# Optimization experiments

Measured on AMD Instinct MI355X. Metric: run time of the kernel, lower is better.

## Reference

```python
import jax, jax.numpy as jnp
import numpy as np

D, B, N, DIM, H, DH, MLP = 6, 4, 1024, 768, 12, 64, 3072
SCALE = DH ** -0.5
EPS = 1e-5


def setup_inputs() -> dict:
    key = jax.random.key(0)
    ks = jax.random.split(key, 5)
    s = 0.02
    return {
        "x": jax.random.normal(ks[0], (B, N, DIM), jnp.float32),
        "ln1_g": jnp.ones((D, DIM), jnp.float32),
        "ln1_b": jnp.zeros((D, DIM), jnp.float32),
        "wqkv": jax.random.normal(ks[1], (D, DIM, 3 * H * DH), jnp.float32) * s,
        "wo": jax.random.normal(ks[2], (D, H * DH, DIM), jnp.float32) * s,
        "bo": jnp.zeros((D, DIM), jnp.float32),
        "ln2_g": jnp.ones((D, DIM), jnp.float32),
        "ln2_b": jnp.zeros((D, DIM), jnp.float32),
        "w1": jax.random.normal(ks[3], (D, DIM, MLP), jnp.float32) * s,
        "b1": jnp.zeros((D, MLP), jnp.float32),
        "w2": jax.random.normal(ks[4], (D, MLP, DIM), jnp.float32) * s,
        "b2": jnp.zeros((D, DIM), jnp.float32),
    }


def _ln(h, g, b):
    m = h.mean(-1, keepdims=True)
    v = h.var(-1, keepdims=True)  # biased, matches torch LayerNorm
    return (h - m) / jnp.sqrt(v + EPS) * g + b


def _heads(t):
    # [b, n, h*d] -> [b, h, n, d]
    return t.reshape(B, N, H, DH).transpose(0, 2, 1, 3)


def reference(x, ln1_g, ln1_b, wqkv, wo, bo, ln2_g, ln2_b, w1, b1, w2, b2):
    def step(carry, p):
        xc, _, _ = carry
        g1, be1, Wqkv, Wo, Bo, g2, be2, W1, B1, W2, B2 = p
        h = _ln(xc, g1, be1)
        q, k, v = jnp.split(h @ Wqkv, 3, axis=-1)
        q, k, v = _heads(q), _heads(k), _heads(v)
        attn = jax.nn.softmax(jnp.einsum('bhid,bhjd->bhij', q, k) * SCALE, axis=-1)
        out = jnp.einsum('bhij,bhjd->bhid', attn, v)
        out = out.transpose(0, 2, 1, 3).reshape(B, N, H * DH)
        xc = xc + out @ Wo + Bo
        h2 = _ln(xc, g2, be2)
        xc = xc + jax.nn.gelu(h2 @ W1 + B1, approximate=False) @ W2 + B2
        return (xc, k, v), None

    kv0 = jnp.zeros((B, H, N, DH), x.dtype)
    (xf, k, v), _ = jax.lax.scan(
        step, (x, kv0, kv0),
        (ln1_g, ln1_b, wqkv, wo, bo, ln2_g, ln2_b, w1, b1, w2, b2))
    return xf, k, v
```

## Files before the change

kernel.cpp:

```cpp
#include <hip/hip_runtime.h>
#include <hip/hip_bf16.h>
#include <math.h>

typedef __bf16 bf16;
typedef __bf16 bf16x8 __attribute__((ext_vector_type(8)));
typedef float f32x4 __attribute__((ext_vector_type(4)));

enum { EPI_QKV = 0, EPI_GELU = 1 };

__device__ __forceinline__ void gload16(const void* g, void* s) {
  __builtin_amdgcn_global_load_lds((__attribute__((address_space(1))) void*)g,
                                   (__attribute__((address_space(3))) void*)s, 16, 0, 0);
}

#define MFMA16(a, b, c) __builtin_amdgcn_mfma_f32_16x16x32_bf16((a), (b), (c), 0, 0, 0)

__device__ __forceinline__ void xcd_swizzle(int& bx, int& by) {
  const int gx = gridDim.x, nwg = gx * gridDim.y;
  int bid = blockIdx.y * gx + blockIdx.x;
  if ((nwg & 7) == 0) bid = (bid & 7) * (nwg >> 3) + (bid >> 3);
  bx = bid % gx;
  by = bid / gx;
}

__global__ __launch_bounds__(256) void cast_x(const float* __restrict__ x,
                                              float* __restrict__ xq) {
  const int i = (blockIdx.x * 256 + threadIdx.x) * 4;
  float4 v = *(const float4*)(x + i);
  v.x = (float)(bf16)v.x; v.y = (float)(bf16)v.y;
  v.z = (float)(bf16)v.z; v.w = (float)(bf16)v.w;
  *(float4*)(xq + i) = v;
}

__global__ __launch_bounds__(256) void wconv_all(
    const float* __restrict__ wqkv, const float* __restrict__ wo,
    const float* __restrict__ w1, const float* __restrict__ w2,
    bf16* __restrict__ qkvT, bf16* __restrict__ woT,
    bf16* __restrict__ w1T, bf16* __restrict__ w2T, int lfix) {
  __shared__ float tile[32][33];
  const int bid = blockIdx.x;
  int l, r;
  if (lfix < 0) { l = bid / 6912; r = bid % 6912; } else { l = lfix; r = bid; }
  const int lo = (lfix < 0) ? l : 0;
  const float* W; bf16* Wt; int K, N, tt;
  if (r < 1728)      { W = wqkv + (size_t)l * 768 * 2304; Wt = qkvT + (size_t)lo * 2304 * 768; K = 768;  N = 2304; tt = r; }
  else if (r < 2304) { W = wo   + (size_t)l * 768 * 768;  Wt = woT  + (size_t)lo * 768 * 768;  K = 768;  N = 768;  tt = r - 1728; }
  else if (r < 4608) { W = w1   + (size_t)l * 768 * 3072; Wt = w1T  + (size_t)lo * 3072 * 768; K = 768;  N = 3072; tt = r - 2304; }
  else               { W = w2   + (size_t)l * 3072 * 768; Wt = w2T  + (size_t)lo * 768 * 3072; K = 3072; N = 768;  tt = r - 4608; }
  const int ntx = N >> 5;
  const int n0 = (tt % ntx) * 32, k0 = (tt / ntx) * 32;
  const int tx = threadIdx.x & 31, ty = threadIdx.x >> 5;
#pragma unroll
  for (int rr = 0; rr < 4; ++rr)
    tile[ty + rr * 8][tx] = W[(size_t)(k0 + ty + rr * 8) * N + n0 + tx];
  __syncthreads();
#pragma unroll
  for (int rr = 0; rr < 4; ++rr)
    Wt[(size_t)(n0 + ty + rr * 8) * K + k0 + tx] = (bf16)tile[tx][ty + rr * 8];
}

__global__ __launch_bounds__(256) void ln_kernel(const float* __restrict__ x,
                                                 const float* __restrict__ g,
                                                 const float* __restrict__ b,
                                                 bf16* __restrict__ out) {
  const int row = blockIdx.x, t = threadIdx.x;
  const float* xr = x + (size_t)row * 768;
  float v0 = xr[t], v1 = xr[t + 256], v2 = xr[t + 512];
  float s = v0 + v1 + v2, sq = v0 * v0 + v1 * v1 + v2 * v2;
#pragma unroll
  for (int m = 32; m; m >>= 1) { s += __shfl_xor(s, m); sq += __shfl_xor(sq, m); }
  __shared__ float rs[4], rq[4];
  const int w = t >> 6;
  if ((t & 63) == 0) { rs[w] = s; rq[w] = sq; }
  __syncthreads();
  s = rs[0] + rs[1] + rs[2] + rs[3];
  sq = rq[0] + rq[1] + rq[2] + rq[3];
  const float mean = s * (1.f / 768.f);
  const float var = sq * (1.f / 768.f) - mean * mean;
  const float rstd = rsqrtf(var + 1e-5f);
  bf16* orow = out + (size_t)row * 768;
  orow[t]       = (bf16)((v0 - mean) * rstd * g[t]       + b[t]);
  orow[t + 256] = (bf16)((v1 - mean) * rstd * g[t + 256] + b[t + 256]);
  orow[t + 512] = (bf16)((v2 - mean) * rstd * g[t + 512] + b[t + 512]);
}

template <int EPI>
__global__ __launch_bounds__(256) void gemm_s(
    const bf16* __restrict__ A, const bf16* __restrict__ Bt,
    const float* __restrict__ bias, bf16* __restrict__ Cb,
    bf16* __restrict__ qo, bf16* __restrict__ ko_, bf16* __restrict__ vo,
    float* __restrict__ kf, float* __restrict__ vf, int wf,
    int M, int Nc, int K) {
  __shared__ __align__(16) char lds[2][2][8192];
  const int t = threadIdx.x, lane = t & 63, w = t >> 6;
  const int wr = w >> 1, wc = w & 1;
  int bx, by;
  xcd_swizzle(bx, by);
  const size_t m0 = (size_t)by * 128, n0 = (size_t)bx * 128;

  const char* ab[2]; const char* bb[2];
#pragma unroll
  for (int r = 0; r < 2; ++r) {
    int c = r * 256 + t;
    ab[r] = (const char*)(A + (m0 + (c >> 2)) * (size_t)K) + (c & 3) * 16;
    bb[r] = (const char*)(Bt + (n0 + (c >> 2)) * (size_t)K) + (c & 3) * 16;
  }

  f32x4 acc[4][4] = {};

  auto stage = [&](int buf, int tt) {
#pragma unroll
    for (int r = 0; r < 2; ++r) {
      gload16(ab[r] + (size_t)tt * 64, &lds[buf][0][r * 4096 + w * 1024]);
      gload16(bb[r] + (size_t)tt * 64, &lds[buf][1][r * 4096 + w * 1024]);
    }
  };
  auto compute = [&](int buf) {
    const char* As = lds[buf][0];
    const char* Bs = lds[buf][1];
    const int ko = (lane >> 4) * 16;
    bf16x8 af[4], fb[4];
#pragma unroll
    for (int i = 0; i < 4; ++i) {
      af[i] = *(const bf16x8*)(As + (wr * 64 + i * 16 + (lane & 15)) * 64 + ko);
      fb[i] = *(const bf16x8*)(Bs + (wc * 64 + i * 16 + (lane & 15)) * 64 + ko);
    }
#pragma unroll
    for (int mi = 0; mi < 4; ++mi)
#pragma unroll
      for (int ni = 0; ni < 4; ++ni)
        acc[mi][ni] = MFMA16(af[mi], fb[ni], acc[mi][ni]);
  };

  const int NT = K >> 5;
  stage(0, 0);
  __syncthreads();
  int cur = 0;
  for (int tt = 1; tt < NT; ++tt) {
    stage(cur ^ 1, tt);
    compute(cur);
    __syncthreads();
    cur ^= 1;
  }
  compute(cur);

#pragma unroll
  for (int mi = 0; mi < 4; ++mi) {
#pragma unroll
    for (int i = 0; i < 4; ++i) {
      size_t row = m0 + wr * 64 + mi * 16 + ((lane >> 4) << 2) + i;
#pragma unroll
      for (int ni = 0; ni < 4; ++ni) {
        size_t col = n0 + wc * 64 + ni * 16 + (lane & 15);
        float v = acc[mi][ni][i];
        if (EPI == EPI_GELU) {
          v += bias[col];
          v = 0.5f * v * (1.f + erff(v * 0.70710678118f));
          Cb[row * (size_t)Nc + col] = (bf16)v;
        } else {
          int b = (int)(row >> 10), n = (int)(row & 1023);
          int which = (int)col >= 1536 ? 2 : ((int)col >= 768 ? 1 : 0);
          int hd = (int)col - which * 768;
          int hh = hd >> 6, d = hd & 63;
          size_t dst = ((size_t)(b * 12 + hh) * 1024 + n) * 64 + d;
          if (which == 0) {
            qo[dst] = (bf16)v;
          } else if (which == 1) {
            ko_[dst] = (bf16)v;
            if (wf) kf[dst] = v;
          } else {
            vo[dst] = (bf16)v;
            if (wf) vf[dst] = v;
          }
        }
      }
    }
  }
}

__global__ __launch_bounds__(256) void gemm64_s(
    const bf16* __restrict__ A, const bf16* __restrict__ Bt,
    const float* __restrict__ bias, const float* __restrict__ res,
    float* __restrict__ Cf, int M, int Nc, int K) {
  __shared__ __align__(16) char lds[2][12288];
  const int t = threadIdx.x, lane = t & 63, w = t >> 6;
  const int wr = w >> 1, wc = w & 1;
  const int l15 = lane & 15, l4 = lane >> 4;
  int bx, by;
  xcd_swizzle(bx, by);
  const size_t m0 = (size_t)by * 64, n0 = (size_t)bx * 128;

  const char* ab = (const char*)(A + (m0 + (t >> 2)) * (size_t)K) + (t & 3) * 16;
  const char* b0 = (const char*)(Bt + (n0 + (t >> 2)) * (size_t)K) + (t & 3) * 16;
  const char* b1 = (const char*)(Bt + (n0 + 64 + (t >> 2)) * (size_t)K) + (t & 3) * 16;

  f32x4 acc[2][4] = {};

  auto stage = [&](int buf, int tt) {
    gload16(ab + (size_t)tt * 64, &lds[buf][t * 16]);
    gload16(b0 + (size_t)tt * 64, &lds[buf][4096 + t * 16]);
    gload16(b1 + (size_t)tt * 64, &lds[buf][8192 + t * 16]);
  };
  auto compute = [&](int buf) {
    const char* L = lds[buf];
    const int ko = l4 * 16;
    bf16x8 fa[2], fb[4];
#pragma unroll
    for (int mi = 0; mi < 2; ++mi)
      fa[mi] = *(const bf16x8*)(L + (wr * 32 + mi * 16 + l15) * 64 + ko);
#pragma unroll
    for (int ni = 0; ni < 4; ++ni)
      fb[ni] = *(const bf16x8*)(L + 4096 + (wc * 64 + ni * 16 + l15) * 64 + ko);
#pragma unroll
    for (int mi = 0; mi < 2; ++mi)
#pragma unroll
      for (int ni = 0; ni < 4; ++ni)
        acc[mi][ni] = MFMA16(fa[mi], fb[ni], acc[mi][ni]);
  };

  const int NT = K >> 5;
  stage(0, 0);
  __syncthreads();
  int cur = 0;
  for (int tt = 1; tt < NT; ++tt) {
    stage(cur ^ 1, tt);
    compute(cur);
    __syncthreads();
    cur ^= 1;
  }
  compute(cur);

#pragma unroll
  for (int mi = 0; mi < 2; ++mi) {
#pragma unroll
    for (int i = 0; i < 4; ++i) {
      size_t row = m0 + wr * 32 + mi * 16 + l4 * 4 + i;
#pragma unroll
      for (int ni = 0; ni < 4; ++ni) {
        size_t col = n0 + wc * 64 + ni * 16 + l15;
        float v = acc[mi][ni][i] + bias[col] + res[row * (size_t)Nc + col];
        Cf[row * (size_t)Nc + col] = v;
      }
    }
  }
}

__global__ __launch_bounds__(256) void vtrans(const bf16* __restrict__ v,
                                              bf16* __restrict__ vT) {
  __shared__ bf16 tile[32][33];
  const int tx = threadIdx.x, ty = threadIdx.y;
  const int bh = blockIdx.x, n0 = blockIdx.y * 32, d0 = blockIdx.z * 32;
  const bf16* vb = v + (size_t)bh * 1024 * 64;
  bf16* vTb = vT + (size_t)bh * 64 * 1024;
#pragma unroll
  for (int r = 0; r < 4; ++r)
    tile[ty + r * 8][tx] = vb[(size_t)(n0 + ty + r * 8) * 64 + d0 + tx];
  __syncthreads();
#pragma unroll
  for (int r = 0; r < 4; ++r)
    vTb[(size_t)(d0 + ty + r * 8) * 1024 + n0 + tx] = tile[tx][ty + r * 8];
}

__global__ __launch_bounds__(64) void attn_kernel(const bf16* __restrict__ q,
                                                  const bf16* __restrict__ k,
                                                  const bf16* __restrict__ vT,
                                                  bf16* __restrict__ out) {
  __shared__ __align__(16) char Ks[16384];
  __shared__ __align__(16) char Vs[16384];
  __shared__ __align__(16) char Ps[8192];
  const int bh = blockIdx.x, qb = blockIdx.y;
  const int lane = threadIdx.x & 63;
  const int l15 = lane & 15, l4 = lane >> 4;

  const char* kp = (const char*)(k + (size_t)bh * 1024 * 64);
  const char* vp = (const char*)(vT + (size_t)bh * 64 * 1024);

  const char* kb0 = kp + (lane >> 3) * 128 + (((lane & 7) ^ ((lane >> 3) & 7)) * 16);
  const int vr0 = lane >> 4;
  const char* vb0 = vp + (size_t)vr0 * 2048 + (((lane & 15) ^ vr0) * 16);
  const char* vb1 = vp + (size_t)(vr0 + 4) * 2048 + (((lane & 15) ^ (vr0 + 4)) * 16);

  bf16x8 aq[2][2];
  {
    const bf16* qbase = q + ((size_t)bh * 1024 + qb * 32) * 64;
#pragma unroll
    for (int mi = 0; mi < 2; ++mi)
#pragma unroll
      for (int ks = 0; ks < 2; ++ks)
        aq[mi][ks] = *(const bf16x8*)(qbase + (mi * 16 + l15) * 64 + ks * 32 + l4 * 8);
  }

  f32x4 oacc[2][4] = {};
  float mrun[2][4], lrun[2][4];
#pragma unroll
  for (int mi = 0; mi < 2; ++mi)
#pragma unroll
    for (int i = 0; i < 4; ++i) { mrun[mi][i] = -1e30f; lrun[mi][i] = 0.f; }

  for (int kb = 0; kb < 8; ++kb) {
    const char* ksrc = kb0 + (size_t)kb * 16384;
#pragma unroll
    for (int r = 0; r < 16; ++r)
      gload16(ksrc + r * 1024, &Ks[r * 1024]);
    const char* vsrc0 = vb0 + kb * 256;
    const char* vsrc1 = vb1 + kb * 256;
#pragma unroll
    for (int r = 0; r < 8; ++r) {
      gload16(vsrc0 + (size_t)r * 16384, &Vs[r * 2048]);
      gload16(vsrc1 + (size_t)r * 16384, &Vs[r * 2048 + 1024]);
    }
    asm volatile("s_waitcnt vmcnt(0)" ::: "memory");

    f32x4 sacc[2][8] = {};
#pragma unroll
    for (int ks = 0; ks < 2; ++ks) {
#pragma unroll
      for (int ni = 0; ni < 8; ++ni) {
        const int rr = ni * 16 + l15;
        const bf16x8 bk = *(const bf16x8*)(Ks + rr * 128 + (((ks * 4 + l4) ^ (rr & 7)) * 16));
        sacc[0][ni] = MFMA16(aq[0][ks], bk, sacc[0][ni]);
        sacc[1][ni] = MFMA16(aq[1][ks], bk, sacc[1][ni]);
      }
    }
#pragma unroll
    for (int mi = 0; mi < 2; ++mi)
#pragma unroll
      for (int ni = 0; ni < 8; ++ni)
        sacc[mi][ni] *= 0.125f;

#pragma unroll
    for (int mi = 0; mi < 2; ++mi) {
#pragma unroll
      for (int i = 0; i < 4; ++i) {
        float mx = sacc[mi][0][i];
#pragma unroll
        for (int ni = 1; ni < 8; ++ni) mx = fmaxf(mx, sacc[mi][ni][i]);
#pragma unroll
        for (int sh = 8; sh; sh >>= 1) mx = fmaxf(mx, __shfl_xor(mx, sh));
        float mnew = fmaxf(mrun[mi][i], mx);
        float alpha = __expf(mrun[mi][i] - mnew);
        mrun[mi][i] = mnew;
        float rsum = 0.f;
#pragma unroll
        for (int ni = 0; ni < 8; ++ni) {
          float pe = __expf(sacc[mi][ni][i] - mnew);
          sacc[mi][ni][i] = pe;
          rsum += pe;
        }
#pragma unroll
        for (int sh = 8; sh; sh >>= 1) rsum += __shfl_xor(rsum, sh);
        lrun[mi][i] = lrun[mi][i] * alpha + rsum;
#pragma unroll
        for (int ni = 0; ni < 4; ++ni) oacc[mi][ni][i] *= alpha;
      }
    }

#pragma unroll
    for (int mi = 0; mi < 2; ++mi)
#pragma unroll
      for (int i = 0; i < 4; ++i) {
        int rowl = mi * 16 + l4 * 4 + i;
        char* prp = Ps + rowl * 256;
        int sw = rowl & 7;
#pragma unroll
        for (int ni = 0; ni < 8; ++ni) {
          int col = ni * 16 + l15;
          *(bf16*)(prp + (((col >> 3) ^ sw) * 16) + (col & 7) * 2) = (bf16)sacc[mi][ni][i];
        }
      }

    const int prow0 = l15, prow1 = 16 + l15;
#pragma unroll
    for (int ks = 0; ks < 4; ++ks) {
      const bf16x8 ap0 = *(const bf16x8*)(Ps + prow0 * 256 + (((ks * 4 + l4) ^ (prow0 & 7)) * 16));
      const bf16x8 ap1 = *(const bf16x8*)(Ps + prow1 * 256 + (((ks * 4 + l4) ^ (prow1 & 7)) * 16));
#pragma unroll
      for (int ni = 0; ni < 4; ++ni) {
        const int vr = ni * 16 + l15;
        const bf16x8 bv = *(const bf16x8*)(Vs + vr * 256 + (((ks * 4 + l4) ^ (vr & 7)) * 16));
        oacc[0][ni] = MFMA16(ap0, bv, oacc[0][ni]);
        oacc[1][ni] = MFMA16(ap1, bv, oacc[1][ni]);
      }
    }
  }

  const int b = bh / 12, hh = bh % 12;
#pragma unroll
  for (int mi = 0; mi < 2; ++mi)
#pragma unroll
    for (int i = 0; i < 4; ++i) {
      int n = qb * 32 + mi * 16 + l4 * 4 + i;
      float inv = 1.f / lrun[mi][i];
      bf16* orow = out + ((size_t)b * 1024 + n) * 768 + hh * 64;
#pragma unroll
      for (int ni = 0; ni < 4; ++ni)
        orow[ni * 16 + l15] = (bf16)(oacc[mi][ni][i] * inv);
    }
}

extern "C" void kernel_launch(void* const* d_in, const int* in_sizes, int n_in,
                              void* d_out, int out_size, void* d_ws, size_t ws_size,
                              hipStream_t stream) {
  (void)in_sizes; (void)n_in; (void)out_size;
  const float* x_in = (const float*)d_in[0];
  const float* ln1g = (const float*)d_in[1];
  const float* ln1b = (const float*)d_in[2];
  const float* wqkv = (const float*)d_in[3];
  const float* wo   = (const float*)d_in[4];
  const float* bo   = (const float*)d_in[5];
  const float* ln2g = (const float*)d_in[6];
  const float* ln2b = (const float*)d_in[7];
  const float* w1   = (const float*)d_in[8];
  const float* b1   = (const float*)d_in[9];
  const float* w2   = (const float*)d_in[10];
  const float* b2   = (const float*)d_in[11];

  float* outx = (float*)d_out;
  float* outk = outx + (size_t)4096 * 768;
  float* outv = outk + (size_t)4096 * 768;

  char* p = (char*)d_ws;
  auto take = [&](size_t bytes) {
    char* r = p;
    p += (bytes + 255) & ~(size_t)255;
    return r;
  };
  float* xw   = (float*)take((size_t)4096 * 768 * 4);
  bf16*  h    = (bf16*)take((size_t)4096 * 768 * 2);
  bf16*  mbuf = (bf16*)take((size_t)4096 * 3072 * 2);
  bf16*  qbuf = (bf16*)take((size_t)4096 * 768 * 2);
  bf16*  kbuf = (bf16*)take((size_t)4096 * 768 * 2);
  bf16*  vbuf = (bf16*)take((size_t)4096 * 768 * 2);
  bf16*  vTb  = (bf16*)take((size_t)4096 * 768 * 2);
  bf16*  abuf = (bf16*)take((size_t)4096 * 768 * 2);

  const size_t wq1 = (size_t)2304 * 768, wo1 = (size_t)768 * 768,
               w11 = (size_t)3072 * 768, w21 = (size_t)768 * 3072;
  const size_t used = (size_t)(p - (char*)d_ws);
  const size_t wbytes = (wq1 + wo1 + w11 + w21) * 2;
  const bool hoist = ws_size >= used + 6 * wbytes + 8192;
  const int nl = hoist ? 6 : 1;
  bf16* qkvT = (bf16*)take(wq1 * 2 * nl);
  bf16* woT  = (bf16*)take(wo1 * 2 * nl);
  bf16* w1T  = (bf16*)take(w11 * 2 * nl);
  bf16* w2T  = (bf16*)take(w21 * 2 * nl);

  cast_x<<<3072, 256, 0, stream>>>(x_in, xw);
  if (hoist)
    wconv_all<<<41472, 256, 0, stream>>>(wqkv, wo, w1, w2, qkvT, woT, w1T, w2T, -1);

  for (int l = 0; l < 6; ++l) {
    if (!hoist)
      wconv_all<<<6912, 256, 0, stream>>>(wqkv, wo, w1, w2, qkvT, woT, w1T, w2T, l);
    bf16* qkL = qkvT + (hoist ? (size_t)l * wq1 : 0);
    bf16* woL = woT  + (hoist ? (size_t)l * wo1 : 0);
    bf16* w1L = w1T  + (hoist ? (size_t)l * w11 : 0);
    bf16* w2L = w2T  + (hoist ? (size_t)l * w21 : 0);

    ln_kernel<<<4096, 256, 0, stream>>>(xw, ln1g + l * 768, ln1b + l * 768, h);
    gemm_s<EPI_QKV><<<dim3(18, 32), 256, 0, stream>>>(
        h, qkL, nullptr, nullptr, qbuf, kbuf, vbuf, outk, outv, l == 5 ? 1 : 0,
        4096, 2304, 768);
    vtrans<<<dim3(48, 32, 2), dim3(32, 8), 0, stream>>>(vbuf, vTb);
    attn_kernel<<<dim3(48, 32), 64, 0, stream>>>(qbuf, kbuf, vTb, abuf);
    gemm64_s<<<dim3(6, 64), 256, 0, stream>>>(
        abuf, woL, bo + l * 768, xw, xw, 4096, 768, 768);
    ln_kernel<<<4096, 256, 0, stream>>>(xw, ln2g + l * 768, ln2b + l * 768, h);
    gemm_s<EPI_GELU><<<dim3(24, 32), 256, 0, stream>>>(
        h, w1L, b1 + l * 3072, mbuf, nullptr, nullptr, nullptr, nullptr, nullptr, 0,
        4096, 3072, 768);
    gemm64_s<<<dim3(6, 64), 256, 0, stream>>>(
        mbuf, w2L, b2 + l * 768, xw, (l == 5) ? outx : xw, 4096, 768, 3072);
  }
}
```

Baseline: 1.283 ms.

## Overlap V loads with QK^T, alias P into K LDS, fold scale, widen weight transpose

The attention kernel now waits only for the K tile before computing QK^T, so the V tile loads overlap with the score computation and softmax; it waits for V just before the PV product. The P buffer reuses the K LDS region, which cuts shared memory per block and may allow more resident blocks. The 1/sqrt(d) scale moves into the QKV GEMM epilogue as an exact power-of-two multiply on Q, which removes per-tile scaling in attention. The weight transpose/convert kernel uses 64x64 tiles with 16-byte bf16x8 stores instead of 32x32 tiles with scalar stores, so it issues fewer, wider writes.

```diff
diff --git a/kernel.cpp b/kernel.cpp
--- a/kernel.cpp
+++ b/kernel.cpp
@@ -37,26 +37,34 @@
     const float* __restrict__ w1, const float* __restrict__ w2,
     bf16* __restrict__ qkvT, bf16* __restrict__ woT,
     bf16* __restrict__ w1T, bf16* __restrict__ w2T, int lfix) {
-  __shared__ float tile[32][33];
-  const int bid = blockIdx.x;
+  __shared__ float tile[64][65];
+  const int bid = blockIdx.x, t = threadIdx.x;
   int l, r;
-  if (lfix < 0) { l = bid / 6912; r = bid % 6912; } else { l = lfix; r = bid; }
+  if (lfix < 0) { l = bid / 1728; r = bid % 1728; } else { l = lfix; r = bid; }
   const int lo = (lfix < 0) ? l : 0;
   const float* W; bf16* Wt; int K, N, tt;
-  if (r < 1728)      { W = wqkv + (size_t)l * 768 * 2304; Wt = qkvT + (size_t)lo * 2304 * 768; K = 768;  N = 2304; tt = r; }
-  else if (r < 2304) { W = wo   + (size_t)l * 768 * 768;  Wt = woT  + (size_t)lo * 768 * 768;  K = 768;  N = 768;  tt = r - 1728; }
-  else if (r < 4608) { W = w1   + (size_t)l * 768 * 3072; Wt = w1T  + (size_t)lo * 3072 * 768; K = 768;  N = 3072; tt = r - 2304; }
-  else               { W = w2   + (size_t)l * 3072 * 768; Wt = w2T  + (size_t)lo * 768 * 3072; K = 3072; N = 768;  tt = r - 4608; }
-  const int ntx = N >> 5;
-  const int n0 = (tt % ntx) * 32, k0 = (tt / ntx) * 32;
-  const int tx = threadIdx.x & 31, ty = threadIdx.x >> 5;
-#pragma unroll
-  for (int rr = 0; rr < 4; ++rr)
-    tile[ty + rr * 8][tx] = W[(size_t)(k0 + ty + rr * 8) * N + n0 + tx];
+  if (r < 432)       { W = wqkv + (size_t)l * 768 * 2304; Wt = qkvT + (size_t)lo * 2304 * 768; K = 768;  N = 2304; tt = r; }
+  else if (r < 576)  { W = wo   + (size_t)l * 768 * 768;  Wt = woT  + (size_t)lo * 768 * 768;  K = 768;  N = 768;  tt = r - 432; }
+  else if (r < 1152) { W = w1   + (size_t)l * 768 * 3072; Wt = w1T  + (size_t)lo * 3072 * 768; K = 768;  N = 3072; tt = r - 576; }
+  else               { W = w2   + (size_t)l * 3072 * 768; Wt = w2T  + (size_t)lo * 768 * 3072; K = 3072; N = 768;  tt = r - 1152; }
+  const int ntx = N >> 6;
+  const int n0 = (tt % ntx) * 64, k0 = (tt / ntx) * 64;
+  const int tx = t & 63, ty = t >> 6;
+#pragma unroll
+  for (int rr = 0; rr < 16; ++rr) {
+    const int row = ty + rr * 4;
+    tile[row][tx] = W[(size_t)(k0 + row) * N + n0 + tx];
+  }
   __syncthreads();
 #pragma unroll
-  for (int rr = 0; rr < 4; ++rr)
-    Wt[(size_t)(n0 + ty + rr * 8) * K + k0 + tx] = (bf16)tile[tx][ty + rr * 8];
+  for (int it = 0; it < 2; ++it) {
+    const int c = it * 256 + t;
+    const int n = c >> 3, kc = (c & 7) * 8;
+    bf16x8 v;
+#pragma unroll
+    for (int j = 0; j < 8; ++j) v[j] = (bf16)tile[kc + j][n];
+    *(bf16x8*)(Wt + (size_t)(n0 + n) * K + k0 + kc) = v;
+  }
 }
 
 __global__ __launch_bounds__(256) void ln_kernel(const float* __restrict__ x,
@@ -164,7 +172,7 @@
           int hh = hd >> 6, d = hd & 63;
           size_t dst = ((size_t)(b * 12 + hh) * 1024 + n) * 64 + d;
           if (which == 0) {
-            qo[dst] = (bf16)v;
+            qo[dst] = (bf16)(v * 0.125f);
           } else if (which == 1) {
             ko_[dst] = (bf16)v;
             if (wf) kf[dst] = v;
@@ -267,7 +275,7 @@
                                                   bf16* __restrict__ out) {
   __shared__ __align__(16) char Ks[16384];
   __shared__ __align__(16) char Vs[16384];
-  __shared__ __align__(16) char Ps[8192];
+  char* Ps = Ks;
   const int bh = blockIdx.x, qb = blockIdx.y;
   const int lane = threadIdx.x & 63;
   const int l15 = lane & 15, l4 = lane >> 4;
@@ -309,7 +317,8 @@
       gload16(vsrc0 + (size_t)r * 16384, &Vs[r * 2048]);
       gload16(vsrc1 + (size_t)r * 16384, &Vs[r * 2048 + 1024]);
     }
-    asm volatile("s_waitcnt vmcnt(0)" ::: "memory");
+    asm volatile("s_waitcnt vmcnt(16)" ::: "memory");
+    __builtin_amdgcn_sched_barrier(0);
 
     f32x4 sacc[2][8] = {};
 #pragma unroll
@@ -322,11 +331,6 @@
         sacc[1][ni] = MFMA16(aq[1][ks], bk, sacc[1][ni]);
       }
     }
-#pragma unroll
-    for (int mi = 0; mi < 2; ++mi)
-#pragma unroll
-      for (int ni = 0; ni < 8; ++ni)
-        sacc[mi][ni] *= 0.125f;
 
 #pragma unroll
     for (int mi = 0; mi < 2; ++mi) {
@@ -368,6 +372,9 @@
           *(bf16*)(prp + (((col >> 3) ^ sw) * 16) + (col & 7) * 2) = (bf16)sacc[mi][ni][i];
         }
       }
+
+    asm volatile("s_waitcnt vmcnt(0)" ::: "memory");
+    __builtin_amdgcn_sched_barrier(0);
 
     const int prow0 = l15, prow1 = 16 + l15;
 #pragma unroll
@@ -447,11 +454,11 @@
 
   cast_x<<<3072, 256, 0, stream>>>(x_in, xw);
   if (hoist)
-    wconv_all<<<41472, 256, 0, stream>>>(wqkv, wo, w1, w2, qkvT, woT, w1T, w2T, -1);
+    wconv_all<<<10368, 256, 0, stream>>>(wqkv, wo, w1, w2, qkvT, woT, w1T, w2T, -1);
 
   for (int l = 0; l < 6; ++l) {
     if (!hoist)
-      wconv_all<<<6912, 256, 0, stream>>>(wqkv, wo, w1, w2, qkvT, woT, w1T, w2T, l);
+      wconv_all<<<1728, 256, 0, stream>>>(wqkv, wo, w1, w2, qkvT, woT, w1T, w2T, l);
     bf16* qkL = qkvT + (hoist ? (size_t)l * wq1 : 0);
     bf16* woL = woT  + (hoist ? (size_t)l * wo1 : 0);
     bf16* w1L = w1T  + (hoist ? (size_t)l * w11 : 0);
```

Measured after the change: 1.294 ms. No clear change (+0.8%).
